# Optimization experiments

Measured on AMD Instinct MI355X. Metric: run time of the kernel, lower is better.

The kernel has to match this reference:

```python
import jax, jax.numpy as jnp
import numpy as np

T, I, H = 4096, 2048, 2048


def setup_inputs() -> dict:
    key = jax.random.key(0)
    ks = jax.random.split(key, 7)
    s = 0.075
    return {
        "x": jax.random.normal(ks[0], (1, T, I), dtype=jnp.float32),
        "W_ih": jax.random.normal(ks[1], (4 * H, I), dtype=jnp.float32) * s,
        "W_hh": jax.random.normal(ks[2], (4 * H, H), dtype=jnp.float32) * s,
        "b_ih": jax.random.normal(ks[3], (4 * H,), dtype=jnp.float32) * s,
        "b_hh": jax.random.normal(ks[4], (4 * H,), dtype=jnp.float32) * s,
        "Wo": jax.random.normal(ks[5], (I, H), dtype=jnp.float32) * s,
        "bo": jax.random.normal(ks[6], (I,), dtype=jnp.float32) * s,
    }


def reference(x, W_ih, W_hh, b_ih, b_hh, Wo, bo):
    xs = x[0]  # [T, I]  (batch dim of 1 squeezed, as in original)
    # Precompute input projections for all timesteps in one big GEMM: [T, 4H]
    gx = xs @ W_ih.T + (b_ih + b_hh)

    def step(carry, gxt):
        h, c = carry  # [H], [H]
        g = gxt + W_hh @ h  # [4H]; PyTorch gate order: i, f, g, o
        i_g, f_g, g_g, o_g = jnp.split(g, 4)
        c_new = jax.nn.sigmoid(f_g) * c + jax.nn.sigmoid(i_g) * jnp.tanh(g_g)
        h_new = jax.nn.sigmoid(o_g) * jnp.tanh(c_new)
        return (h_new, c_new), h_new

    h0 = jnp.zeros((H,), dtype=x.dtype)
    c0 = jnp.zeros((H,), dtype=x.dtype)
    _, hs = jax.lax.scan(step, (h0, c0), gx)  # hs: [T, H]

    out = jax.nn.sigmoid(hs @ Wo.T + bo)  # [T, I]
    return out[None]  # [1, T, I]
```

## Files before the change

### kernel.cpp

```cpp
#include <hip/hip_runtime.h>

#define T_STEPS 4096
#define IDIM 2048
#define HDIM 2048
#define G4DIM 8192

typedef __attribute__((ext_vector_type(8))) short short8;
typedef __attribute__((ext_vector_type(4))) float f32x4;
typedef __attribute__((ext_vector_type(2))) float f32x2;

__device__ __forceinline__ unsigned short f2bf(float f) {
  unsigned int u = __float_as_uint(f);
  u += 0x7fffu + ((u >> 16) & 1u);
  return (unsigned short)(u >> 16);
}
__device__ __forceinline__ float bf2f(unsigned short h) {
  return __uint_as_float(((unsigned int)h) << 16);
}

template <int ACT_SIGMOID, int OUT_BF16>
__global__ __launch_bounds__(256) void gemm_bt(
    const float* __restrict__ A, const float* __restrict__ B,
    const float* __restrict__ bias, void* __restrict__ Cout,
    int M, int N, int K)
{
  __shared__ short Ah[64][40];
  __shared__ short Al[64][40];
  __shared__ short Bh[64][40];
  __shared__ short Bl[64][40];
  const int tid  = threadIdx.x;
  const int wave = tid >> 6, lane = tid & 63;
  const int bn = blockIdx.x * 64, bm = blockIdx.y * 64;
  const int srow = tid >> 2, sc8 = (tid & 3) * 8;
  const int wm = (wave >> 1) * 32, wn = (wave & 1) * 32;
  const int lq = lane >> 4, lr = lane & 15;
  f32x4 acc[2][2] = {};

  for (int k0 = 0; k0 < K; k0 += 32) {
    __syncthreads();
    {
      const float* src = A + (size_t)(bm + srow) * K + k0 + sc8;
      float4 v0 = *(const float4*)(src);
      float4 v1 = *(const float4*)(src + 4);
      float vv[8] = {v0.x, v0.y, v0.z, v0.w, v1.x, v1.y, v1.z, v1.w};
      short8 vh, vl;
      #pragma unroll
      for (int i = 0; i < 8; ++i) {
        unsigned short hb = f2bf(vv[i]);
        vh[i] = (short)hb;
        vl[i] = (short)f2bf(vv[i] - bf2f(hb));
      }
      *(short8*)&Ah[srow][sc8] = vh;
      *(short8*)&Al[srow][sc8] = vl;
    }
    {
      const float* src = B + (size_t)(bn + srow) * K + k0 + sc8;
      float4 v0 = *(const float4*)(src);
      float4 v1 = *(const float4*)(src + 4);
      float vv[8] = {v0.x, v0.y, v0.z, v0.w, v1.x, v1.y, v1.z, v1.w};
      short8 vh, vl;
      #pragma unroll
      for (int i = 0; i < 8; ++i) {
        unsigned short hb = f2bf(vv[i]);
        vh[i] = (short)hb;
        vl[i] = (short)f2bf(vv[i] - bf2f(hb));
      }
      *(short8*)&Bh[srow][sc8] = vh;
      *(short8*)&Bl[srow][sc8] = vl;
    }
    __syncthreads();

    short8 ah0 = *(const short8*)&Ah[wm +      lr][lq * 8];
    short8 al0 = *(const short8*)&Al[wm +      lr][lq * 8];
    short8 ah1 = *(const short8*)&Ah[wm + 16 + lr][lq * 8];
    short8 al1 = *(const short8*)&Al[wm + 16 + lr][lq * 8];
    short8 bh0 = *(const short8*)&Bh[wn +      lr][lq * 8];
    short8 bl0 = *(const short8*)&Bl[wn +      lr][lq * 8];
    short8 bh1 = *(const short8*)&Bh[wn + 16 + lr][lq * 8];
    short8 bl1 = *(const short8*)&Bl[wn + 16 + lr][lq * 8];

    acc[0][0] = __builtin_amdgcn_mfma_f32_16x16x32_bf16(ah0, bh0, acc[0][0], 0, 0, 0);
    acc[0][0] = __builtin_amdgcn_mfma_f32_16x16x32_bf16(ah0, bl0, acc[0][0], 0, 0, 0);
    acc[0][0] = __builtin_amdgcn_mfma_f32_16x16x32_bf16(al0, bh0, acc[0][0], 0, 0, 0);

    acc[0][1] = __builtin_amdgcn_mfma_f32_16x16x32_bf16(ah0, bh1, acc[0][1], 0, 0, 0);
    acc[0][1] = __builtin_amdgcn_mfma_f32_16x16x32_bf16(ah0, bl1, acc[0][1], 0, 0, 0);
    acc[0][1] = __builtin_amdgcn_mfma_f32_16x16x32_bf16(al0, bh1, acc[0][1], 0, 0, 0);

    acc[1][0] = __builtin_amdgcn_mfma_f32_16x16x32_bf16(ah1, bh0, acc[1][0], 0, 0, 0);
    acc[1][0] = __builtin_amdgcn_mfma_f32_16x16x32_bf16(ah1, bl0, acc[1][0], 0, 0, 0);
    acc[1][0] = __builtin_amdgcn_mfma_f32_16x16x32_bf16(al1, bh0, acc[1][0], 0, 0, 0);

    acc[1][1] = __builtin_amdgcn_mfma_f32_16x16x32_bf16(ah1, bh1, acc[1][1], 0, 0, 0);
    acc[1][1] = __builtin_amdgcn_mfma_f32_16x16x32_bf16(ah1, bl1, acc[1][1], 0, 0, 0);
    acc[1][1] = __builtin_amdgcn_mfma_f32_16x16x32_bf16(al1, bh1, acc[1][1], 0, 0, 0);
  }

  #pragma unroll
  for (int mi = 0; mi < 2; ++mi) {
    #pragma unroll
    for (int ni = 0; ni < 2; ++ni) {
      #pragma unroll
      for (int rr = 0; rr < 4; ++rr) {
        int row = bm + wm + mi * 16 + lq * 4 + rr;
        int col = bn + wn + ni * 16 + lr;
        float v = acc[mi][ni][rr];
        if (bias) v += bias[col];
        if (ACT_SIGMOID) v = 1.f / (1.f + __expf(-v));
        if (OUT_BF16)
          ((unsigned short*)Cout)[(size_t)row * N + col] = f2bf(v);
        else
          ((float*)Cout)[(size_t)row * N + col] = v;
      }
    }
  }
}

__global__ __launch_bounds__(1024, 4) void lstm_scan(
    const float* __restrict__ Whh,
    const float* __restrict__ b_ih, const float* __restrict__ b_hh,
    const unsigned short* __restrict__ gx,
    float* __restrict__ hs)
{
  const int b   = blockIdx.x;
  const int tid = threadIdx.x;
  const int u   = tid & 7;
  const int kc  = tid >> 3;
  const int wv  = tid >> 6;

  f32x2 w2[4][8];
  #pragma unroll
  for (int g = 0; g < 4; ++g) {
    const float* wp = Whh + (size_t)(g * HDIM + b * 8 + u) * HDIM + kc * 16;
    #pragma unroll
    for (int i = 0; i < 4; ++i) {
      float4 v = *(const float4*)(wp + 4 * i);
      w2[g][2 * i]     = f32x2{v.x, v.y};
      w2[g][2 * i + 1] = f32x2{v.z, v.w};
    }
  }
  float bias_r = 0.f;
  if (tid < 32) {
    int br = (tid >> 3) * HDIM + b * 8 + (tid & 7);
    bias_r = b_ih[br] + b_hh[br];
  }
  float cval = 0.f;

  __shared__ float h_lds[128 * 20];
  __shared__ float partials[2][32][18];
  unsigned int* hs_u = (unsigned int*)hs;

  const unsigned short* gxp = gx + (tid >> 3) * HDIM + b * 8 + (tid & 7);
  unsigned short gxr_cur = 0, gxr_nxt = 0;
  if (tid < 32) gxr_cur = gxp[0];

  for (int t = 0; t < T_STEPS; ++t) {
    const int buf = t & 1;
    if (tid < 32 && t + 1 < T_STEPS)
      gxr_nxt = gxp[(size_t)(t + 1) * G4DIM];

    f32x2 h2w;
    if (t > 0) {
      const unsigned long long* p =
          (const unsigned long long*)(hs_u + (size_t)(t - 1) * HDIM + tid * 2);
      for (;;) {
        unsigned long long v =
            __hip_atomic_load(p, __ATOMIC_RELAXED, __HIP_MEMORY_SCOPE_AGENT);
        unsigned int lo = (unsigned int)v, hi = (unsigned int)(v >> 32);
        if (lo != 0xAAAAAAAAu && hi != 0xAAAAAAAAu) {
          h2w = f32x2{__uint_as_float(lo), __uint_as_float(hi)};
          break;
        }
        __builtin_amdgcn_s_sleep(1);
      }
    } else {
      h2w = f32x2{0.f, 0.f};
    }

    *(f32x2*)&h_lds[kc * 20 + u * 2] = h2w;

    f32x2 acc0{0.f, 0.f}, acc1{0.f, 0.f}, acc2{0.f, 0.f}, acc3{0.f, 0.f};
    #pragma unroll
    for (int i = 0; i < 4; ++i) {
      float4 hv = *(const float4*)&h_lds[kc * 20 + i * 4];
      f32x2 ha{hv.x, hv.y}, hb{hv.z, hv.w};
      acc0 += w2[0][2 * i] * ha;  acc0 += w2[0][2 * i + 1] * hb;
      acc1 += w2[1][2 * i] * ha;  acc1 += w2[1][2 * i + 1] * hb;
      acc2 += w2[2][2 * i] * ha;  acc2 += w2[2][2 * i + 1] * hb;
      acc3 += w2[3][2 * i] * ha;  acc3 += w2[3][2 * i + 1] * hb;
    }
    float s0 = acc0[0] + acc0[1];
    float s1 = acc1[0] + acc1[1];
    float s2 = acc2[0] + acc2[1];
    float s3 = acc3[0] + acc3[1];
    #pragma unroll
    for (int m = 8; m <= 32; m <<= 1) {
      s0 += __shfl_xor(s0, m, 64);
      s1 += __shfl_xor(s1, m, 64);
      s2 += __shfl_xor(s2, m, 64);
      s3 += __shfl_xor(s3, m, 64);
    }
    if ((tid & 56) == 0) {
      partials[buf][0 * 8 + u][wv] = s0;
      partials[buf][1 * 8 + u][wv] = s1;
      partials[buf][2 * 8 + u][wv] = s2;
      partials[buf][3 * 8 + u][wv] = s3;
    }
    __syncthreads();

    if (tid < 64) {
      __builtin_amdgcn_s_setprio(1);
      float gval = 0.f;
      if (tid < 32) {
        float s = bf2f(gxr_cur) + bias_r;
        const float* pr = &partials[buf][tid][0];
        #pragma unroll
        for (int i = 0; i < 8; ++i) {
          float2 v = *(const float2*)(pr + 2 * i);
          s += v.x + v.y;
        }
        gval = s;
      }
      float g_i = __shfl(gval, tid);
      float g_f = __shfl(gval, tid + 8);
      float g_g = __shfl(gval, tid + 16);
      float g_o = __shfl(gval, tid + 24);
      if (tid < 8) {
        float is = 1.f / (1.f + __expf(-g_i));
        float fs = 1.f / (1.f + __expf(-g_f));
        float os = 1.f / (1.f + __expf(-g_o));
        float e2 = __expf(-2.f * fabsf(g_g));
        float tg = (1.f - e2) / (1.f + e2);
        tg = (g_g < 0.f) ? -tg : tg;
        float cn = fs * cval + is * tg;
        cval = cn;
        float ec = __expf(-2.f * fabsf(cn));
        float tc = (1.f - ec) / (1.f + ec);
        tc = (cn < 0.f) ? -tc : tc;
        float hn = os * tc;
        __hip_atomic_store(hs_u + (size_t)t * HDIM + b * 8 + tid,
                           __float_as_uint(hn),
                           __ATOMIC_RELAXED, __HIP_MEMORY_SCOPE_AGENT);
      }
      __builtin_amdgcn_s_setprio(0);
    }
    gxr_cur = gxr_nxt;
  }
}

extern "C" void kernel_launch(void* const* d_in, const int* in_sizes, int n_in,
                              void* d_out, int out_size, void* d_ws, size_t ws_size,
                              hipStream_t stream) {
  (void)in_sizes; (void)n_in; (void)out_size; (void)ws_size;
  const float* x    = (const float*)d_in[0];
  const float* W_ih = (const float*)d_in[1];
  const float* W_hh = (const float*)d_in[2];
  const float* b_ih = (const float*)d_in[3];
  const float* b_hh = (const float*)d_in[4];
  const float* Wo   = (const float*)d_in[5];
  const float* bo   = (const float*)d_in[6];
  float* out = (float*)d_out;

  char* ws = (char*)d_ws;
  unsigned short* gx = (unsigned short*)ws;
  float* hs = (float*)(ws + (size_t)T_STEPS * G4DIM * 2);

  hipMemsetAsync(hs, 0xAA, (size_t)T_STEPS * HDIM * sizeof(float), stream);

  gemm_bt<0, 1><<<dim3(G4DIM / 64, T_STEPS / 64), 256, 0, stream>>>(
      x, W_ih, nullptr, gx, T_STEPS, G4DIM, IDIM);

  lstm_scan<<<256, 1024, 0, stream>>>(W_hh, b_ih, b_hh, gx, hs);

  gemm_bt<1, 0><<<dim3(IDIM / 64, T_STEPS / 64), 256, 0, stream>>>(
      hs, Wo, bo, out, T_STEPS, IDIM, HDIM);
}
```

Before: 11.84 ms.

## Replace per-element sentinel polling with per-step counter flags and LDS token broadcast

Instead of every thread spinning on the hs values until no 0xAAAAAAAA sentinel remains, each block bumps a per-step counter (one per group of 8 blocks) after writing its h slice. Only wave 0 polls the 32 counters; it then publishes a workgroup-scope token in LDS that the other waves wait on before doing a plain load of h. This cuts global polling traffic across 256 blocks × 1024 threads and drops the large sentinel memset. In exchange it adds an extra acquire/release hop and an intra-block token handoff on the critical path of each timestep, and it depends on the release fetch-add correctly ordering the h stores made by other lanes.

```diff
diff --git a/kernel.cpp b/kernel.cpp
--- a/kernel.cpp
+++ b/kernel.cpp
@@ -120,13 +120,15 @@
     const float* __restrict__ Whh,
     const float* __restrict__ b_ih, const float* __restrict__ b_hh,
     const unsigned short* __restrict__ gx,
-    float* __restrict__ hs)
+    float* __restrict__ hs,
+    int* __restrict__ cnt)
 {
-  const int b   = blockIdx.x;
-  const int tid = threadIdx.x;
-  const int u   = tid & 7;
-  const int kc  = tid >> 3;
-  const int wv  = tid >> 6;
+  const int b    = blockIdx.x;
+  const int tid  = threadIdx.x;
+  const int u    = tid & 7;
+  const int kc   = tid >> 3;
+  const int wv   = tid >> 6;
+  const int lane = tid & 63;
 
   f32x2 w2[4][8];
   #pragma unroll
@@ -148,6 +150,8 @@
 
   __shared__ float h_lds[128 * 20];
   __shared__ float partials[2][32][18];
+  __shared__ int   token;
+  if (tid == 0) token = 0;
   unsigned int* hs_u = (unsigned int*)hs;
 
   const unsigned short* gxp = gx + (tid >> 3) * HDIM + b * 8 + (tid & 7);
@@ -161,18 +165,27 @@
 
     f32x2 h2w;
     if (t > 0) {
-      const unsigned long long* p =
-          (const unsigned long long*)(hs_u + (size_t)(t - 1) * HDIM + tid * 2);
-      for (;;) {
-        unsigned long long v =
-            __hip_atomic_load(p, __ATOMIC_RELAXED, __HIP_MEMORY_SCOPE_AGENT);
-        unsigned int lo = (unsigned int)v, hi = (unsigned int)(v >> 32);
-        if (lo != 0xAAAAAAAAu && hi != 0xAAAAAAAAu) {
-          h2w = f32x2{__uint_as_float(lo), __uint_as_float(hi)};
-          break;
+      if (wv == 0) {
+        const int* cp = cnt + (size_t)(t - 1) * 32;
+        for (;;) {
+          int v = 8;
+          if (lane < 32)
+            v = __hip_atomic_load(cp + lane, __ATOMIC_RELAXED,
+                                  __HIP_MEMORY_SCOPE_AGENT);
+          if (__all(v == 8)) break;
+          __builtin_amdgcn_s_sleep(1);
         }
-        __builtin_amdgcn_s_sleep(1);
-      }
+        __builtin_amdgcn_fence(__ATOMIC_ACQUIRE, "agent");
+        __hip_atomic_store(&token, t, __ATOMIC_RELEASE,
+                           __HIP_MEMORY_SCOPE_WORKGROUP);
+      } else {
+        while (__hip_atomic_load(&token, __ATOMIC_RELAXED,
+                                 __HIP_MEMORY_SCOPE_WORKGROUP) < t)
+          __builtin_amdgcn_s_sleep(1);
+        __builtin_amdgcn_fence(__ATOMIC_ACQUIRE, "workgroup");
+      }
+      float2 hv = *(const float2*)(hs + (size_t)(t - 1) * HDIM + tid * 2);
+      h2w = f32x2{hv.x, hv.y};
     } else {
       h2w = f32x2{0.f, 0.f};
     }
@@ -242,6 +255,9 @@
                            __float_as_uint(hn),
                            __ATOMIC_RELAXED, __HIP_MEMORY_SCOPE_AGENT);
       }
+      if (tid == 0)
+        __hip_atomic_fetch_add(cnt + (size_t)t * 32 + (b >> 3), 1,
+                               __ATOMIC_RELEASE, __HIP_MEMORY_SCOPE_AGENT);
       __builtin_amdgcn_s_setprio(0);
     }
     gxr_cur = gxr_nxt;
@@ -264,13 +280,15 @@
   char* ws = (char*)d_ws;
   unsigned short* gx = (unsigned short*)ws;
   float* hs = (float*)(ws + (size_t)T_STEPS * G4DIM * 2);
-
-  hipMemsetAsync(hs, 0xAA, (size_t)T_STEPS * HDIM * sizeof(float), stream);
+  int*  cnt = (int*)(ws + (size_t)T_STEPS * G4DIM * 2
+                        + (size_t)T_STEPS * HDIM * 4);
+
+  hipMemsetAsync(cnt, 0, (size_t)T_STEPS * 32 * sizeof(int), stream);
 
   gemm_bt<0, 1><<<dim3(G4DIM / 64, T_STEPS / 64), 256, 0, stream>>>(
       x, W_ih, nullptr, gx, T_STEPS, G4DIM, IDIM);
 
-  lstm_scan<<<256, 1024, 0, stream>>>(W_hh, b_ih, b_hh, gx, hs);
+  lstm_scan<<<256, 1024, 0, stream>>>(W_hh, b_ih, b_hh, gx, hs, cnt);
 
   gemm_bt<1, 0><<<dim3(IDIM / 64, T_STEPS / 64), 256, 0, stream>>>(
       hs, Wo, bo, out, T_STEPS, IDIM, HDIM);
```

New measurement: 30.89 ms. +161.0%, slower.
